# Kernel optimization log

Hardware: AMD Instinct MI355X
Metric: run time of the kernel (lower is better)

Reference implementation:

```python
import jax, jax.numpy as jnp
import numpy as np

GAMMA = 10.0   # RBF width of the stand-in radial kernel
EPS = 1e-12    # safe-norm epsilon (avoids NaN grad at zero difference)

N_POINTS = 16384
N_NBR = 32
C_IN = 16
C_OUT = 16
N_BASIS = 16


def setup_inputs() -> dict:
    key = jax.random.key(0)
    k1, k2, k3, k4, k5, k6 = jax.random.split(key, 6)
    inp = jax.random.normal(k1, (C_IN, N_POINTS), dtype=jnp.float32)
    coords = jax.random.normal(k2, (N_POINTS, 3), dtype=jnp.float32)
    W = jax.random.normal(k3, (C_OUT, C_IN, N_BASIS), dtype=jnp.float32)
    centers = jax.random.uniform(k4, (N_BASIS,), dtype=jnp.float32)
    relative_mask = jax.random.uniform(k5, (N_POINTS, N_NBR), dtype=jnp.float32)
    neighbors = jax.random.randint(k6, (N_POINTS, N_NBR), 0, N_POINTS)
    return {"input": inp, "coords": coords, "W": W, "centers": centers,
            "relative_mask": relative_mask, "neighbors": neighbors}


def reference(input, coords, W, centers, relative_mask, neighbors):
    # difference_matrix: [N, K, 3]
    diff = coords[neighbors] - coords[:, None, :]
    # edge length with safe sqrt: [N, K]
    r = jnp.sqrt(jnp.sum(diff * diff, axis=-1) + EPS)
    # Gaussian radial basis: [N, K, B]
    rbf = jnp.exp(-GAMMA * (r[..., None] - centers) ** 2)
    # per-edge kernel: [C_out, C_in, N, K]
    kernel = jnp.einsum('oib,nkb->oink', W, rbf)
    # relative_mask applied as einsum 'ba,dcba->dcba'
    kernel = relative_mask * kernel
    # neighbor feature gather: [C_in, N, K]
    neighbors_input = input[:, neighbors]
    # contraction 'cba,dcba->db': [C_out, N]
    output = jnp.einsum('ink,oink->on', neighbors_input, kernel)
    return output
```

## Files before the change

kernel.cpp:

```cpp
#include <hip/hip_runtime.h>
#include <hip/hip_bf16.h>

#define NPTS 16384
#define NNBR 32
#define CIN 16
#define COUT 16
#define NBASIS 16

#define WF_OS 264
#define ML_PS 264

typedef _Float16 half8 __attribute__((ext_vector_type(8)));
typedef _Float16 half4 __attribute__((ext_vector_type(4)));
typedef unsigned short ushort8 __attribute__((ext_vector_type(8)));
typedef float floatx4 __attribute__((ext_vector_type(4)));

#define WS_XT 0
#define WS_WF (NPTS * CIN)

__global__ __launch_bounds__(256) void prep_kernel(
        const float* __restrict__ input, const float* __restrict__ W,
        _Float16* __restrict__ ws) {
    const int p4 = threadIdx.x >> 2;
    const int c4 = threadIdx.x & 3;
    const int n = blockIdx.x * 64 + p4;
    half4 v;
    #pragma unroll
    for (int j = 0; j < 4; ++j)
        v[j] = (_Float16)input[(c4 * 4 + j) * NPTS + n];
    *(half4*)&ws[WS_XT + n * CIN + c4 * 4] = v;
    if (blockIdx.x == 0) {
        const int o = threadIdx.x >> 4, b = threadIdx.x & 15;
        _Float16 w[16];
        #pragma unroll
        for (int i = 0; i < CIN; ++i) w[i] = (_Float16)W[o * 256 + i * 16 + b];
        *(half8*)&ws[WS_WF + o * 256 + b * 16]     = *(half8*)&w[0];
        *(half8*)&ws[WS_WF + o * 256 + b * 16 + 8] = *(half8*)&w[8];
    }
}

__global__ __launch_bounds__(256, 8) void se3_conv_kernel(
        const _Float16* __restrict__ ws,
        const float* __restrict__ coords,
        const float* __restrict__ centers,
        const float* __restrict__ mask,
        const int* __restrict__ neighbors,
        float* __restrict__ out) {
    __shared__ _Float16 Wf[COUT * WF_OS];
    __shared__ _Float16 Mld[8 * ML_PS];
    __shared__ float    rs[8 * NNBR];
    __shared__ unsigned short nb16[8 * NNBR];
    __shared__ _Float16 mv16[8 * NNBR];

    const _Float16* xT16 = &ws[WS_XT];

    const int tid = threadIdx.x;
    const int t = tid & 15;
    const int quad = (tid >> 4) & 3;
    const int wv = tid >> 6;
    const int nbase = blockIdx.x * 8;

    {
        const int o = tid >> 4, ch = tid & 15;
        const half8 w0 = *(const half8*)&ws[WS_WF + o * 256 + ch * 16];
        const half8 w1 = *(const half8*)&ws[WS_WF + o * 256 + ch * 16 + 8];
        *(half8*)&Wf[o * WF_OS + ch * 16]     = w0;
        *(half8*)&Wf[o * WF_OS + ch * 16 + 8] = w1;
    }

    {
        const int pt = tid >> 5;
        const int k = tid & 31;
        const int n = nbase + pt;
        const int nbr = neighbors[n * NNBR + k] & (NPTS - 1);
        const float m = mask[n * NNBR + k];
        const float dx = coords[nbr * 3 + 0] - coords[n * 3 + 0];
        const float dy = coords[nbr * 3 + 1] - coords[n * 3 + 1];
        const float dz = coords[nbr * 3 + 2] - coords[n * 3 + 2];
        rs[pt * NNBR + k] = sqrtf(dx * dx + dy * dy + dz * dz + 1e-12f);
        nb16[pt * NNBR + k] = (unsigned short)nbr;
        mv16[pt * NNBR + k] = (_Float16)m;
    }
    __syncthreads();

    const float cb = centers[t];
    #pragma unroll
    for (int q = 0; q < 2; ++q) {
        const int pq = wv * 2 + q;
        const int kb = pq * NNBR + 8 * quad;
        const float4 r0 = *(const float4*)&rs[kb];
        const float4 r1 = *(const float4*)&rs[kb + 4];
        const ushort8 nbv = *(const ushort8*)&nb16[kb];
        const half8 mvv = *(const half8*)&mv16[kb];
        const float rj[8] = {r0.x, r0.y, r0.z, r0.w, r1.x, r1.y, r1.z, r1.w};
        half8 af, bf;
        #pragma unroll
        for (int j = 0; j < 8; ++j) {
            const float d = rj[j] - cb;
            bf[j] = (_Float16)__expf(-10.0f * d * d);
            const float x = (float)xT16[(int)nbv[j] * CIN + t];
            af[j] = (_Float16)(x * (float)mvv[j]);
        }
        floatx4 c = {0.0f, 0.0f, 0.0f, 0.0f};
        c = __builtin_amdgcn_mfma_f32_16x16x32_f16(af, bf, c, 0, 0, 0);
        _Float16 h[4];
        #pragma unroll
        for (int v = 0; v < 4; ++v) h[v] = (_Float16)c[v];
        *(uint2*)&Mld[pq * ML_PS + t * 16 + 4 * quad] = *(uint2*)h;
    }
    __syncthreads();

    floatx4 acc = {0.0f, 0.0f, 0.0f, 0.0f};
    #pragma unroll
    for (int cch = 0; cch < 8; ++cch) {
        const int bi = cch * 32 + 8 * quad;
        const half8 a = *(const half8*)&Wf[t * WF_OS + bi];
        half8 b = {};
        if (t < 8) b = *(const half8*)&Mld[t * ML_PS + bi];
        acc = __builtin_amdgcn_mfma_f32_16x16x32_f16(a, b, acc, 0, 0, 0);
    }
    if (t < 8 && wv == (t >> 1)) {
        #pragma unroll
        for (int v = 0; v < 4; ++v)
            out[(4 * quad + v) * NPTS + nbase + t] = acc[v];
    }
}

extern "C" void kernel_launch(void* const* d_in, const int* in_sizes, int n_in,
                              void* d_out, int out_size, void* d_ws, size_t ws_size,
                              hipStream_t stream) {
    const float* input   = (const float*)d_in[0];
    const float* coords  = (const float*)d_in[1];
    const float* W       = (const float*)d_in[2];
    const float* centers = (const float*)d_in[3];
    const float* mask    = (const float*)d_in[4];
    const int*   nbr     = (const int*)d_in[5];
    float* out = (float*)d_out;
    _Float16* ws = (_Float16*)d_ws;

    prep_kernel<<<NPTS / 64, 256, 0, stream>>>(input, W, ws);
    se3_conv_kernel<<<NPTS / 8, 256, 0, stream>>>(ws, coords, centers, mask,
                                                  nbr, out);
}
```

Baseline: 74.69 us.

## Fuse prep and conv into one persistent cooperative kernel with grid sync

Replaces the two launches (input transpose/convert prep and the conv kernel) with a single persistent cooperative kernel. Each block converts W into shared memory itself, transposes its share of the input, waits on a grid-wide barrier, then loops over point tiles. The aim is to remove the second launch and the inter-kernel gap. In exchange it adds a grid sync, redundant per-block W conversion, and an extra __syncthreads per tile, and it depends on cooperative launch support, falling back to the old path otherwise.

```diff
diff --git a/kernel.cpp b/kernel.cpp
--- a/kernel.cpp
+++ b/kernel.cpp
@@ -1,11 +1,12 @@
 #include <hip/hip_runtime.h>
-#include <hip/hip_bf16.h>
+#include <hip/hip_cooperative_groups.h>
 
 #define NPTS 16384
 #define NNBR 32
 #define CIN 16
 #define COUT 16
 #define NBASIS 16
+#define NTILES (NPTS / 8)
 
 #define WF_OS 264
 #define ML_PS 264
@@ -17,6 +18,114 @@
 
 #define WS_XT 0
 #define WS_WF (NPTS * CIN)
+
+__global__ __launch_bounds__(256, 8) void se3_fused_kernel(
+        const float* __restrict__ input,
+        const float* __restrict__ coords,
+        const float* __restrict__ W,
+        const float* __restrict__ centers,
+        const float* __restrict__ mask,
+        const int* __restrict__ neighbors,
+        float* __restrict__ out,
+        _Float16* __restrict__ ws) {
+    __shared__ _Float16 Wf[COUT * WF_OS];
+    __shared__ _Float16 Mld[8 * ML_PS];
+    __shared__ float    rs[8 * NNBR];
+    __shared__ unsigned short nb16[8 * NNBR];
+    __shared__ _Float16 mv16[8 * NNBR];
+
+    const int tid = threadIdx.x;
+    const int t = tid & 15;
+    const int quad = (tid >> 4) & 3;
+    const int wv = tid >> 6;
+
+    {
+        const int o = tid >> 4, b = tid & 15;
+        _Float16 w[16];
+        #pragma unroll
+        for (int i = 0; i < CIN; ++i) w[i] = (_Float16)W[o * 256 + i * 16 + b];
+        *(half8*)&Wf[o * WF_OS + b * 16]     = *(half8*)&w[0];
+        *(half8*)&Wf[o * WF_OS + b * 16 + 8] = *(half8*)&w[8];
+    }
+
+    for (int tile = blockIdx.x; tile < NTILES; tile += gridDim.x) {
+        if (tid < 32) {
+            const int p = tid >> 2, c4 = tid & 3;
+            const int n = tile * 8 + p;
+            half4 v;
+            #pragma unroll
+            for (int j = 0; j < 4; ++j)
+                v[j] = (_Float16)input[(c4 * 4 + j) * NPTS + n];
+            *(half4*)&ws[WS_XT + n * CIN + c4 * 4] = v;
+        }
+    }
+
+    const _Float16* xT16 = &ws[WS_XT];
+    const float cb = centers[t];
+
+    __threadfence();
+    cooperative_groups::this_grid().sync();
+
+    for (int tile = blockIdx.x; tile < NTILES; tile += gridDim.x) {
+        const int nbase = tile * 8;
+
+        {
+            const int pt = tid >> 5;
+            const int k = tid & 31;
+            const int n = nbase + pt;
+            const int nbr = neighbors[n * NNBR + k] & (NPTS - 1);
+            const float m = mask[n * NNBR + k];
+            const float dx = coords[nbr * 3 + 0] - coords[n * 3 + 0];
+            const float dy = coords[nbr * 3 + 1] - coords[n * 3 + 1];
+            const float dz = coords[nbr * 3 + 2] - coords[n * 3 + 2];
+            rs[pt * NNBR + k] = sqrtf(dx * dx + dy * dy + dz * dz + 1e-12f);
+            nb16[pt * NNBR + k] = (unsigned short)nbr;
+            mv16[pt * NNBR + k] = (_Float16)m;
+        }
+
+        #pragma unroll
+        for (int q = 0; q < 2; ++q) {
+            const int pq = wv * 2 + q;
+            const int kb = pq * NNBR + 8 * quad;
+            const float4 r0 = *(const float4*)&rs[kb];
+            const float4 r1 = *(const float4*)&rs[kb + 4];
+            const ushort8 nbv = *(const ushort8*)&nb16[kb];
+            const half8 mvv = *(const half8*)&mv16[kb];
+            const float rj[8] = {r0.x, r0.y, r0.z, r0.w, r1.x, r1.y, r1.z, r1.w};
+            half8 af, bf;
+            #pragma unroll
+            for (int j = 0; j < 8; ++j) {
+                const float d = rj[j] - cb;
+                bf[j] = (_Float16)__expf(-10.0f * d * d);
+                const float x = (float)xT16[(int)nbv[j] * CIN + t];
+                af[j] = (_Float16)(x * (float)mvv[j]);
+            }
+            floatx4 c = {0.0f, 0.0f, 0.0f, 0.0f};
+            c = __builtin_amdgcn_mfma_f32_16x16x32_f16(af, bf, c, 0, 0, 0);
+            _Float16 h[4];
+            #pragma unroll
+            for (int v = 0; v < 4; ++v) h[v] = (_Float16)c[v];
+            *(uint2*)&Mld[pq * ML_PS + t * 16 + 4 * quad] = *(uint2*)h;
+        }
+        __syncthreads();
+
+        floatx4 acc = {0.0f, 0.0f, 0.0f, 0.0f};
+        #pragma unroll
+        for (int cch = 0; cch < 8; ++cch) {
+            const int bi = cch * 32 + 8 * quad;
+            const half8 a = *(const half8*)&Wf[t * WF_OS + bi];
+            half8 b = {};
+            if (t < 8) b = *(const half8*)&Mld[t * ML_PS + bi];
+            acc = __builtin_amdgcn_mfma_f32_16x16x32_f16(a, b, acc, 0, 0, 0);
+        }
+        if (t < 8 && wv == (t >> 1)) {
+            #pragma unroll
+            for (int v = 0; v < 4; ++v)
+                out[(4 * quad + v) * NPTS + nbase + t] = acc[v];
+        }
+        __syncthreads();
+    }
+}
 
 __global__ __launch_bounds__(256) void prep_kernel(
         const float* __restrict__ input, const float* __restrict__ W,
@@ -138,6 +247,32 @@
     float* out = (float*)d_out;
     _Float16* ws = (_Float16*)d_ws;
 
+    static int coop_grid = -1;
+    if (coop_grid < 0) {
+        int dev = 0;
+        (void)hipGetDevice(&dev);
+        int nCU = 0;
+        if (hipDeviceGetAttribute(&nCU, hipDeviceAttributeMultiprocessorCount,
+                                  dev) != hipSuccess) nCU = 0;
+        int maxb = 0;
+        if (hipOccupancyMaxActiveBlocksPerMultiprocessor(&maxb, se3_fused_kernel,
+                                                         256, 0) != hipSuccess)
+            maxb = 0;
+        const long long cap = (long long)maxb * (long long)nCU;
+        coop_grid = (cap >= 256) ? (int)((cap < NTILES) ? cap : NTILES) : 0;
+        (void)hipGetLastError();
+    }
+
+    if (coop_grid > 0) {
+        void* args[] = {(void*)&input, (void*)&coords, (void*)&W, (void*)&centers,
+                        (void*)&mask, (void*)&nbr, (void*)&out, (void*)&ws};
+        if (hipLaunchCooperativeKernel(se3_fused_kernel, dim3(coop_grid),
+                                       dim3(256), args, 0, stream) == hipSuccess)
+            return;
+        coop_grid = 0;
+        (void)hipGetLastError();
+    }
+
     prep_kernel<<<NPTS / 64, 256, 0, stream>>>(input, W, ws);
     se3_conv_kernel<<<NPTS / 8, 256, 0, stream>>>(ws, coords, centers, mask,
                                                   nbr, out);
```

After: 202.1 us. 171% more time.
